# Performance work log

Hardware: AMD Instinct MI355X
Metric: run time of the kernel (lower is better)

## Reference

```python
import jax, jax.numpy as jnp
import numpy as np
from jax import lax

KERNEL_EPS = 1e-4   # eps in softmax_kernel
ATTN_EPS = 1e-6     # eps in causal_linear_attention
CHUNK = 64          # chunk length for the causal scan


def softmax_kernel(data, projection_matrix, is_query):
    # data: [b,h,n,d], projection_matrix: [r,d]
    d = data.shape[-1]
    r = projection_matrix.shape[0]
    data_normalizer = d ** -0.25
    ratio = r ** -0.5
    data_dash = jnp.einsum('bhnd,rd->bhnr', data_normalizer * data, projection_matrix)
    diag_data = (jnp.sum(data ** 2, axis=-1) * 0.5 * data_normalizer ** 2)[..., None]  # [b,h,n,1]
    if is_query:
        stab = jnp.max(data_dash, axis=-1, keepdims=True)
    else:
        stab = jnp.max(data_dash)
    return ratio * (jnp.exp(data_dash - diag_data - stab) + KERNEL_EPS)


def causal_linear_attention(qp, kp, v, chunk=CHUNK, eps=ATTN_EPS):
    # qp,kp: [b,h,n,r] feature maps; v: [b,h,n,e]
    b, h, n, r = qp.shape
    e = v.shape[-1]
    nc = n // chunk
    # -> [nc, b, h, chunk, *] for lax.scan over chunks
    qs = jnp.moveaxis(qp.reshape(b, h, nc, chunk, r), 2, 0)
    ks = jnp.moveaxis(kp.reshape(b, h, nc, chunk, r), 2, 0)
    vs = jnp.moveaxis(v.reshape(b, h, nc, chunk, e), 2, 0)

    def step(carry, xs):
        k_last, ctx_last = carry  # [b,h,r], [b,h,r,e]
        qch, kch, vch = xs        # [b,h,c,r], [b,h,c,r], [b,h,c,e]
        k_cum = k_last[:, :, None, :] + jnp.cumsum(kch, axis=2)              # [b,h,c,r]
        D_inv = 1.0 / jnp.einsum('bhcr,bhcr->bhc', qch, k_cum + eps)         # [b,h,c]
        ctx = jnp.einsum('bhcr,bhce->bhcre', kch, vch)                       # [b,h,c,r,e]
        ctx_cum = ctx_last[:, :, None] + jnp.cumsum(ctx, axis=2)             # [b,h,c,r,e]
        out = jnp.einsum('bhcre,bhcr,bhc->bhce', ctx_cum, qch, D_inv)        # [b,h,c,e]
        return (k_cum[:, :, -1], ctx_cum[:, :, -1]), out

    init = (jnp.zeros((b, h, r), qp.dtype), jnp.zeros((b, h, r, e), qp.dtype))
    _, outs = lax.scan(step, init, (qs, ks, vs))  # outs: [nc,b,h,c,e]
    return jnp.moveaxis(outs, 0, 2).reshape(b, h, n, e)


def setup_inputs() -> dict:
    key = jax.random.key(0)
    kq, kk, kv, kp = jax.random.split(key, 4)
    b, h, n, d, r = 2, 8, 4096, 64, 256
    q = jax.random.normal(kq, (b, h, n, d), dtype=jnp.float32)
    k = jax.random.normal(kk, (b, h, n, d), dtype=jnp.float32)
    v = jax.random.normal(kv, (b, h, n, d), dtype=jnp.float32)
    projection_matrix = jax.random.normal(kp, (r, d), dtype=jnp.float32)
    return {"q": q, "k": k, "v": v, "projection_matrix": projection_matrix}


def reference(q, k, v, projection_matrix):
    qp = softmax_kernel(q, projection_matrix, is_query=True)
    kp = softmax_kernel(k, projection_matrix, is_query=False)
    return causal_linear_attention(qp, kp, v)
```

## Files before the change

### kernel.cpp

```cpp
#include <hip/hip_runtime.h>


typedef unsigned short ushort_t;
typedef __attribute__((ext_vector_type(8))) short bf16x8;
typedef __attribute__((ext_vector_type(4))) float f32x4;

#define KEPS 1e-4f
#define AEPS 1e-6f
#define NORMIZER 0.35355339059327373f
#define RATIO 0.0625f

__device__ __forceinline__ ushort_t bf16r(float f) {
  unsigned u = __float_as_uint(f);
  return (ushort_t)((u + 0x7fffu + ((u >> 16) & 1u)) >> 16);
}
__device__ __forceinline__ float ubf(ushort_t h) {
  return __uint_as_float((unsigned)h << 16);
}

__global__ __launch_bounds__(256) void pconv_kernel(
    const float* __restrict__ P, ushort_t* __restrict__ Phi,
    ushort_t* __restrict__ Plo)
{
  int idx = blockIdx.x * 1024 + threadIdx.x;
  #pragma unroll
  for (int p = 0; p < 4; ++p) {
    int i = idx + p * 256;
    float x = P[i];
    ushort_t h = bf16r(x);
    Phi[i] = h;
    Plo[i] = bf16r(x - ubf(h));
  }
}

__device__ __forceinline__ void stage_ptile(const ushort_t* __restrict__ gt,
                                            ushort_t* lds0, int tid) {
  int wv = tid >> 6, lane = tid & 63;
  #pragma unroll
  for (int i = 0; i < 2; ++i) {
    int D = i * 256 + wv * 64 + lane;
    int row = D >> 3, c3 = D & 7;
    int sc = (row << 3) | (c3 ^ (row & 7));
    __builtin_amdgcn_global_load_lds(
        (const __attribute__((address_space(1))) void*)(gt + sc * 8),
        (__attribute__((address_space(3))) void*)(lds0 + (i * 256 + wv * 64) * 8),
        16, 0, 0);
  }
}

__global__ __launch_bounds__(256, 4) void feat_mfma(
    const float* __restrict__ Q, const float* __restrict__ K,
    const float* __restrict__ V,
    const ushort_t* __restrict__ Phi, const ushort_t* __restrict__ Plo,
    ushort_t* __restrict__ qp, ushort_t* __restrict__ E,
    float* __restrict__ bmax,
    ushort_t* __restrict__ SE, float* __restrict__ zE,
    float* __restrict__ SV)
{
  __shared__ union {
    struct {
      ushort_t Xhi[64 * 72];
      ushort_t Xlo[64 * 72];
      ushort_t Pt[2][4096];
    } s;
    ushort_t outb[64 * 268];
    ushort_t Et[256 * 72];
  } u;
  __shared__ float diagS[64];
  __shared__ float redm[4];

  int bid = blockIdx.x, tid = threadIdx.x;
  bool isK = bid < 1024;
  int bc = bid;
  const float* X = isK ? K : Q;
  size_t rowbase = (size_t)(isK ? bid : bid - 1024) * 64;

  int lane = tid & 63, wv = tid >> 6;
  int n15 = lane & 15, quad = lane >> 4;

  stage_ptile(Phi, &u.s.Pt[0][0], tid);

  float vraw[16];
  if (isK) {
    #pragma unroll
    for (int ks = 0; ks < 2; ++ks)
      #pragma unroll
      for (int jj = 0; jj < 8; ++jj) {
        int pos = quad * 8 + 32 * ks + jj;
        vraw[ks * 8 + jj] = V[rowbase * 64 + (size_t)pos * 64 + 16 * wv + n15];
      }
  }

  #pragma unroll
  for (int p = 0; p < 4; ++p) {
    int idx = tid + p * 256;
    int row = idx >> 4, c4 = idx & 15;
    float4 x = *(const float4*)&X[(rowbase + row) * 64 + c4 * 4];
    ushort4 h, l;
    h.x = bf16r(x.x); l.x = bf16r(x.x - ubf(h.x));
    h.y = bf16r(x.y); l.y = bf16r(x.y - ubf(h.y));
    h.z = bf16r(x.z); l.z = bf16r(x.z - ubf(h.z));
    h.w = bf16r(x.w); l.w = bf16r(x.w - ubf(h.w));
    *(ushort4*)&u.s.Xhi[row * 72 + c4 * 4] = h;
    *(ushort4*)&u.s.Xlo[row * 72 + c4 * 4] = l;
    float ss = x.x * x.x + x.y * x.y + x.z * x.z + x.w * x.w;
    ss += __shfl_xor(ss, 1, 64); ss += __shfl_xor(ss, 2, 64);
    ss += __shfl_xor(ss, 4, 64); ss += __shfl_xor(ss, 8, 64);
    if ((tid & 15) == 0) diagS[row] = 0.0625f * ss;
  }

  bf16x8 aV[2];
  if (isK) {
    float vsum = 0.f;
    #pragma unroll
    for (int ks = 0; ks < 2; ++ks)
      #pragma unroll
      for (int jj = 0; jj < 8; ++jj) {
        float x = vraw[ks * 8 + jj];
        vsum += x;
        aV[ks][jj] = (short)bf16r(x);
      }
    vsum += __shfl_xor(vsum, 16, 64);
    vsum += __shfl_xor(vsum, 32, 64);
    if (quad == 0) SV[(size_t)bc * 64 + 16 * wv + n15] = vsum;
  }

  __syncthreads();

  bf16x8 ah[2], al[2];
  #pragma unroll
  for (int ks = 0; ks < 2; ++ks) {
    int off = (16 * wv + n15) * 72 + quad * 8 + 32 * ks;
    ah[ks] = *(const bf16x8*)&u.s.Xhi[off];
    al[ks] = *(const bf16x8*)&u.s.Xlo[off];
  }

  f32x4 acc[16];
  #pragma unroll
  for (int tc = 0; tc < 16; ++tc) acc[tc] = f32x4{0.f, 0.f, 0.f, 0.f};

  int buf = 0;
  #pragma unroll
  for (int t = 0; t < 8; ++t) {
    int q4 = t >> 1;
    bool isLo = t & 1;
    if (t) {
      asm volatile("s_waitcnt vmcnt(0)" ::: "memory");
      __builtin_amdgcn_s_barrier();
    }
    if (t < 7) {
      int tn = t + 1;
      const ushort_t* gt = ((tn & 1) ? Plo : Phi) + (size_t)(tn >> 1) * 4096;
      stage_ptile(gt, &u.s.Pt[buf ^ 1][0], tid);
    }
    #pragma unroll
    for (int tcl = 0; tcl < 4; ++tcl) {
      f32x4 a = acc[q4 * 4 + tcl];
      #pragma unroll
      for (int ks = 0; ks < 2; ++ks) {
        int jr = 16 * tcl + n15;
        int rc = (quad + 4 * ks) ^ (n15 & 7);
        bf16x8 b = *(const bf16x8*)&u.s.Pt[buf][jr * 64 + rc * 8];
        a = __builtin_amdgcn_mfma_f32_16x16x32_bf16(ah[ks], b, a, 0, 0, 0);
        if (!isLo)
          a = __builtin_amdgcn_mfma_f32_16x16x32_bf16(al[ks], b, a, 0, 0, 0);
      }
      acc[q4 * 4 + tcl] = a;
    }
    buf ^= 1;
  }

  float dg[4];
  #pragma unroll
  for (int r = 0; r < 4; ++r) dg[r] = diagS[16 * wv + quad * 4 + r];

  float sub[4];
  if (!isK) {
    #pragma unroll
    for (int r = 0; r < 4; ++r) {
      float mx = -3.0e38f;
      #pragma unroll
      for (int tc = 0; tc < 16; ++tc) mx = fmaxf(mx, acc[tc][r]);
      #pragma unroll
      for (int s = 1; s < 16; s <<= 1) mx = fmaxf(mx, __shfl_xor(mx, s, 64));
      sub[r] = dg[r] + NORMIZER * mx;
    }
  } else {
    float bm = -3.0e38f;
    #pragma unroll
    for (int tc = 0; tc < 16; ++tc)
      #pragma unroll
      for (int r = 0; r < 4; ++r) bm = fmaxf(bm, acc[tc][r]);
    #pragma unroll
    for (int s = 1; s < 64; s <<= 1) bm = fmaxf(bm, __shfl_xor(bm, s, 64));
    if (lane == 0) redm[wv] = bm;
    #pragma unroll
    for (int r = 0; r < 4; ++r) sub[r] = dg[r];
  }

  unsigned hp[16][2];
  __syncthreads();
  ushort_t* dst = (isK ? E : qp) + rowbase * 256;
  #pragma unroll
  for (int tc = 0; tc < 16; ++tc) {
    #pragma unroll
    for (int r = 0; r < 4; ++r) {
      int row = 16 * wv + quad * 4 + r;
      float ex = __expf(NORMIZER * acc[tc][r] - sub[r]);
      float val = isK ? ex : RATIO * (ex + KEPS);
      ushort_t h = bf16r(val);
      u.outb[row * 268 + 16 * tc + n15] = h;
      if (r & 1) hp[tc][r >> 1] |= ((unsigned)h << 16);
      else       hp[tc][r >> 1] = (unsigned)h;
    }
  }
  __syncthreads();
  #pragma unroll
  for (int p = 0; p < 8; ++p) {
    int g = (tid + p * 256) * 8;
    int row = g >> 8, c0 = g & 255;
    bf16x8 v0 = *(const bf16x8*)&u.outb[row * 268 + c0];
    *(bf16x8*)&dst[row * 256 + c0] = v0;
  }

  if (isK && tid == 0) {
    float m4 = fmaxf(fmaxf(redm[0], redm[1]), fmaxf(redm[2], redm[3]));
    bmax[bc] = NORMIZER * m4;
  }

  if (!isK) return;

  __syncthreads();

  #pragma unroll
  for (int tc = 0; tc < 16; ++tc) {
    int j = 16 * tc + n15;
    int rot = 8 * ((j >> 3) & 7);
    int pw = (16 * wv + quad * 4 + rot) & 63;
    ushort4 w4;
    w4.x = (ushort_t)(hp[tc][0] & 0xffffu);
    w4.y = (ushort_t)(hp[tc][0] >> 16);
    w4.z = (ushort_t)(hp[tc][1] & 0xffffu);
    w4.w = (ushort_t)(hp[tc][1] >> 16);
    *(ushort4*)&u.Et[j * 72 + pw] = w4;
  }
  __syncthreads();

  {
    float s = 0.f;
    #pragma unroll
    for (int m8 = 0; m8 < 8; ++m8) {
      bf16x8 r8 = *(const bf16x8*)&u.Et[tid * 72 + m8 * 8];
      #pragma unroll
      for (int x = 0; x < 8; ++x) s += ubf((ushort_t)r8[x]);
    }
    zE[(size_t)bc * 256 + tid] = s;
  }

  f32x4 acc2[16];
  #pragma unroll
  for (int tc = 0; tc < 16; ++tc) {
    int j = 16 * tc + n15;
    int rot = 8 * ((j >> 3) & 7);
    f32x4 a = {0.f, 0.f, 0.f, 0.f};
    #pragma unroll
    for (int ks = 0; ks < 2; ++ks) {
      int pr = (quad * 8 + 32 * ks + rot) & 63;
      bf16x8 b = *(const bf16x8*)&u.Et[j * 72 + pr];
      a = __builtin_amdgcn_mfma_f32_16x16x32_bf16(aV[ks], b, a, 0, 0, 0);
    }
    acc2[tc] = a;
  }
  __syncthreads();

  #pragma unroll
  for (int tc = 0; tc < 16; ++tc)
    #pragma unroll
    for (int r = 0; r < 4; ++r) {
      int e = 16 * wv + quad * 4 + r;
      u.outb[e * 268 + 16 * tc + n15] = bf16r(acc2[tc][r]);
    }
  __syncthreads();
  ushort_t* sdst = SE + rowbase * 256;
  #pragma unroll
  for (int p = 0; p < 8; ++p) {
    int g = (tid + p * 256) * 8;
    int e = g >> 8, j0 = g & 255;
    bf16x8 v0 = *(const bf16x8*)&u.outb[e * 268 + j0];
    *(bf16x8*)&sdst[e * 256 + j0] = v0;
  }
}

__global__ __launch_bounds__(256) void kmax_reduce(
    const float* __restrict__ bmax, float* __restrict__ kmax)
{
  __shared__ float red[4];
  int tid = threadIdx.x;
  float m = fmaxf(fmaxf(bmax[tid], bmax[tid + 256]),
                  fmaxf(bmax[tid + 512], bmax[tid + 768]));
  #pragma unroll
  for (int s = 1; s < 64; s <<= 1) m = fmaxf(m, __shfl_xor(m, s, 64));
  if ((tid & 63) == 0) red[tid >> 6] = m;
  __syncthreads();
  if (tid == 0)
    *kmax = fmaxf(fmaxf(red[0], red[1]), fmaxf(red[2], red[3]));
}

__global__ __launch_bounds__(256) void prefix_kernel(
    ushort_t* __restrict__ S, float* __restrict__ zE,
    const float* __restrict__ SV, const float* __restrict__ kmax)
{
  int b = blockIdx.x;
  float m = *kmax;
  float c1 = RATIO * __expf(-m);
  const float c0 = RATIO * KEPS;
  if (b < 1024) {
    int flat = b * 256 + threadIdx.x;
    int bh = flat >> 14;
    int idx = flat & 16383;
    int e = idx >> 8;
    size_t base = (size_t)bh * 1048576 + idx;
    const float* svp = SV + (size_t)bh * 4096 + e;
    float runE = 0.f, runV = 0.f;
    for (int cc = 0; cc < 64; cc += 8) {
      ushort_t t[8]; float sv[8];
      #pragma unroll
      for (int u2 = 0; u2 < 8; ++u2) {
        t[u2] = S[base + (size_t)(cc + u2) * 16384];
        sv[u2] = svp[(size_t)(cc + u2) * 64];
      }
      #pragma unroll
      for (int u2 = 0; u2 < 8; ++u2) {
        S[base + (size_t)(cc + u2) * 16384] = bf16r(c1 * runE + c0 * runV);
        runE += ubf(t[u2]);
        runV += sv[u2];
      }
    }
  } else {
    int bh = b - 1024;
    int j = threadIdx.x;
    size_t base = (size_t)bh * 16384 + j;
    float run = 0.f;
    for (int cc = 0; cc < 64; cc += 8) {
      float t[8];
      #pragma unroll
      for (int u2 = 0; u2 < 8; ++u2)
        t[u2] = zE[base + (size_t)(cc + u2) * 256];
      #pragma unroll
      for (int u2 = 0; u2 < 8; ++u2) {
        zE[base + (size_t)(cc + u2) * 256] = run;
        run += c1 * t[u2] + 64.0f * c0;
      }
    }
  }
}

__device__ __forceinline__ void stage_tile(const ushort_t* __restrict__ gt,
                                           ushort_t* lds0, int tid, int wv) {
  #pragma unroll
  for (int i = 0; i < 2; ++i) {
    int D = i * 256 + tid;
    int row = D >> 5, cl = D & 31;
    int sc = (row << 5) | (cl ^ (row & 7));
    __builtin_amdgcn_global_load_lds(
        (const __attribute__((address_space(1))) void*)(gt + sc * 8),
        (__attribute__((address_space(3))) void*)(lds0 + (i * 256 + wv * 64) * 8),
        16, 0, 0);
  }
}

__global__ __launch_bounds__(256) void fused_mfma(
    const ushort_t* __restrict__ qp, const ushort_t* __restrict__ E,
    const float* __restrict__ kmax, const float* __restrict__ Z,
    const ushort_t* __restrict__ S, const float* __restrict__ V,
    float* __restrict__ out)
{
  __shared__ ushort_t As[64 * 72];
  __shared__ ushort_t Vt[64 * 72];
  __shared__ ushort_t Bst[2][4096];
  __shared__ float zv[256];
  __shared__ float qsumS[64];
  __shared__ float dqS[64];

  int bc = blockIdx.x, tid = threadIdx.x;
  int lane = tid & 63, wv = tid >> 6;
  int n15 = lane & 15, quad = lane >> 4;
  float m = *kmax;
  float c1 = RATIO * __expf(-m);
  const float c0 = RATIO * KEPS;
  size_t base = (size_t)bc * 16384;

  zv[tid] = Z[(size_t)bc * 256 + tid] + AEPS;
  #pragma unroll
  for (int p = 0; p < 16; ++p) {
    int idx = tid + p * 256;
    int t = idx >> 6, e = idx & 63;
    Vt[e * 72 + t] = bf16r(V[(size_t)bc * 4096 + idx]);
  }
  __syncthreads();

  stage_tile(E + base, &Bst[0][0], tid, wv);

  bf16x8 aQ[8];
  #pragma unroll
  for (int ks = 0; ks < 8; ++ks)
    aQ[ks] = *(const bf16x8*)&qp[base + (size_t)(16 * wv + n15) * 256 + quad * 8 + 32 * ks];

  float qsum = 0.f, dq = 0.f;
  #pragma unroll
  for (int ks = 0; ks < 8; ++ks)
    #pragma unroll
    for (int j = 0; j < 8; ++j) {
      float qv = ubf((ushort_t)aQ[ks][j]);
      qsum += qv;
      dq += qv * zv[quad * 8 + 32 * ks + j];
    }
  qsum += __shfl_xor(qsum, 16, 64); qsum += __shfl_xor(qsum, 32, 64);
  dq   += __shfl_xor(dq, 16, 64);   dq   += __shfl_xor(dq, 32, 64);
  if (quad == 0) { qsumS[16 * wv + n15] = qsum; dqS[16 * wv + n15] = dq; }

  float rs[4] = {0.f, 0.f, 0.f, 0.f};
  float dinv[4] = {0.f, 0.f, 0.f, 0.f};

  #pragma unroll
  for (int t = 0; t < 8; ++t) {
    asm volatile("s_waitcnt vmcnt(0)" ::: "memory");
    __builtin_amdgcn_s_barrier();
    if (t < 7) {
      const ushort_t* gt = (t < 3) ? (E + base + (size_t)(t + 1) * 4096)
                                   : (S + base + (size_t)(t - 3) * 4096);
      stage_tile(gt, &Bst[(t + 1) & 1][0], tid, wv);
    }

    bf16x8 bf[8];
    #pragma unroll
    for (int ks = 0; ks < 8; ++ks) {
      int rc = (4 * ks + quad) ^ (n15 & 7);
      bf[ks] = *(const bf16x8*)&Bst[t & 1][(n15 * 32 + rc) * 8];
    }
    f32x4 g = {0.f, 0.f, 0.f, 0.f};
    #pragma unroll
    for (int ks = 0; ks < 8; ++ks)
      g = __builtin_amdgcn_mfma_f32_16x16x32_bf16(aQ[ks], bf[ks], g, 0, 0, 0);

    if (t < 4) {
      int tc = t;
      #pragma unroll
      for (int r = 0; r < 4; ++r) {
        int i = 16 * wv + quad * 4 + r;
        int tt = 16 * tc + n15;
        float val = (tt <= i) ? (c1 * g[r] + c0 * qsumS[i]) : 0.f;
        As[i * 72 + tt] = bf16r(val);
        rs[r] += val;
      }
      if (t == 3) {
        #pragma unroll
        for (int r = 0; r < 4; ++r) {
          float v2 = rs[r];
          #pragma unroll
          for (int s = 1; s < 16; s <<= 1) v2 += __shfl_xor(v2, s, 64);
          int i = 16 * wv + quad * 4 + r;
          dinv[r] = 1.f / (dqS[i] + v2);
        }
      }
    } else {
      int ec = t - 4;
      f32x4 o = g;
      #pragma unroll
      for (int ks = 0; ks < 2; ++ks) {
        bf16x8 a2 = *(const bf16x8*)&As[(16 * wv + n15) * 72 + quad * 8 + 32 * ks];
        bf16x8 b2 = *(const bf16x8*)&Vt[(16 * ec + n15) * 72 + quad * 8 + 32 * ks];
        o = __builtin_amdgcn_mfma_f32_16x16x32_bf16(a2, b2, o, 0, 0, 0);
      }
      #pragma unroll
      for (int r = 0; r < 4; ++r) {
        int i = 16 * wv + quad * 4 + r;
        out[(size_t)bc * 4096 + (size_t)i * 64 + 16 * ec + n15] = o[r] * dinv[r];
      }
    }
  }
}

extern "C" void kernel_launch(void* const* d_in, const int* in_sizes, int n_in,
                              void* d_out, int out_size, void* d_ws, size_t ws_size,
                              hipStream_t stream)
{
  const float* q = (const float*)d_in[0];
  const float* k = (const float*)d_in[1];
  const float* v = (const float*)d_in[2];
  const float* P = (const float*)d_in[3];
  float* out = (float*)d_out;

  ushort_t* qp  = (ushort_t*)d_ws;
  ushort_t* E   = qp + 16777216;
  ushort_t* S   = E + 16777216;
  float*    zE  = (float*)(S + 16777216);
  float*    SV  = zE + 262144;
  ushort_t* Phi = (ushort_t*)(SV + 65536);
  ushort_t* Plo = Phi + 16384;
  float*    bmax = (float*)(Plo + 16384);
  float*    kmax = bmax + 1024;

  pconv_kernel<<<16, 256, 0, stream>>>(P, Phi, Plo);
  feat_mfma<<<2048, 256, 0, stream>>>(q, k, v, Phi, Plo, qp, E, bmax,
                                      S, zE, SV);
  kmax_reduce<<<1, 256, 0, stream>>>(bmax, kmax);
  prefix_kernel<<<1040, 256, 0, stream>>>(S, zE, SV, kmax);
  fused_mfma<<<1024, 256, 0, stream>>>(qp, E, kmax, zE, S, v, out);
}
```

Baseline: 157.5 us.

## Drop kmax kernel, load X directly to registers, use packed bf16 converts

Removes the single-block kmax_reduce launch and instead has every prefix and fused block recompute the global max from the 1024 per-block maxima. In feat_mfma the X tile now goes straight from global memory into MFMA operand registers instead of passing through LDS as hi/lo arrays. Scalar bf16 rounding is replaced with the hardware v_cvt_pk_bf16_f32 instruction throughout. The intent is to cut a kernel launch and its serialization, LDS traffic and ALU work. The cost is redundant reads of bmax in every block and possibly less coalesced X loads.

```diff
diff --git a/kernel.cpp b/kernel.cpp
--- a/kernel.cpp
+++ b/kernel.cpp
@@ -17,6 +17,12 @@
 __device__ __forceinline__ float ubf(ushort_t h) {
   return __uint_as_float((unsigned)h << 16);
 }
+__device__ __forceinline__ unsigned cvtpk(float lo, float hi) {
+  unsigned r;
+  asm("v_cvt_pk_bf16_f32 %0, %1, %2" : "=v"(r) : "v"(lo), "v"(hi));
+  return r;
+}
+union U32V { unsigned u[4]; bf16x8 v; };
 
 __global__ __launch_bounds__(256) void pconv_kernel(
     const float* __restrict__ P, ushort_t* __restrict__ Phi,
@@ -58,11 +64,7 @@
     float* __restrict__ SV)
 {
   __shared__ union {
-    struct {
-      ushort_t Xhi[64 * 72];
-      ushort_t Xlo[64 * 72];
-      ushort_t Pt[2][4096];
-    } s;
+    ushort_t Pt[2][4096];
     ushort_t outb[64 * 268];
     ushort_t Et[256 * 72];
   } u;
@@ -78,7 +80,7 @@
   int lane = tid & 63, wv = tid >> 6;
   int n15 = lane & 15, quad = lane >> 4;
 
-  stage_ptile(Phi, &u.s.Pt[0][0], tid);
+  stage_ptile(Phi, &u.Pt[0][0], tid);
 
   float vraw[16];
   if (isK) {
@@ -91,49 +93,64 @@
       }
   }
 
-  #pragma unroll
-  for (int p = 0; p < 4; ++p) {
-    int idx = tid + p * 256;
-    int row = idx >> 4, c4 = idx & 15;
-    float4 x = *(const float4*)&X[(rowbase + row) * 64 + c4 * 4];
-    ushort4 h, l;
-    h.x = bf16r(x.x); l.x = bf16r(x.x - ubf(h.x));
-    h.y = bf16r(x.y); l.y = bf16r(x.y - ubf(h.y));
-    h.z = bf16r(x.z); l.z = bf16r(x.z - ubf(h.z));
-    h.w = bf16r(x.w); l.w = bf16r(x.w - ubf(h.w));
-    *(ushort4*)&u.s.Xhi[row * 72 + c4 * 4] = h;
-    *(ushort4*)&u.s.Xlo[row * 72 + c4 * 4] = l;
-    float ss = x.x * x.x + x.y * x.y + x.z * x.z + x.w * x.w;
-    ss += __shfl_xor(ss, 1, 64); ss += __shfl_xor(ss, 2, 64);
-    ss += __shfl_xor(ss, 4, 64); ss += __shfl_xor(ss, 8, 64);
-    if ((tid & 15) == 0) diagS[row] = 0.0625f * ss;
+  float xr[2][8];
+  {
+    const float* Xr = X + (rowbase + 16 * wv + n15) * 64;
+    #pragma unroll
+    for (int ks = 0; ks < 2; ++ks) {
+      float4 a = *(const float4*)&Xr[quad * 8 + 32 * ks];
+      float4 b = *(const float4*)&Xr[quad * 8 + 32 * ks + 4];
+      xr[ks][0] = a.x; xr[ks][1] = a.y; xr[ks][2] = a.z; xr[ks][3] = a.w;
+      xr[ks][4] = b.x; xr[ks][5] = b.y; xr[ks][6] = b.z; xr[ks][7] = b.w;
+    }
+  }
+  {
+    float ss = 0.f;
+    #pragma unroll
+    for (int ks = 0; ks < 2; ++ks)
+      #pragma unroll
+      for (int j = 0; j < 8; ++j) ss += xr[ks][j] * xr[ks][j];
+    ss += __shfl_xor(ss, 16, 64);
+    ss += __shfl_xor(ss, 32, 64);
+    if (quad == 0) diagS[16 * wv + n15] = 0.0625f * ss;
+  }
+
+  bf16x8 ah[2], al[2];
+  #pragma unroll
+  for (int ks = 0; ks < 2; ++ks) {
+    U32V H, L;
+    #pragma unroll
+    for (int j2 = 0; j2 < 4; ++j2)
+      H.u[j2] = cvtpk(xr[ks][2 * j2], xr[ks][2 * j2 + 1]);
+    #pragma unroll
+    for (int j2 = 0; j2 < 4; ++j2) {
+      float r0 = xr[ks][2 * j2]     - __uint_as_float(H.u[j2] << 16);
+      float r1 = xr[ks][2 * j2 + 1] - __uint_as_float(H.u[j2] & 0xffff0000u);
+      L.u[j2] = cvtpk(r0, r1);
+    }
+    ah[ks] = H.v;
+    al[ks] = L.v;
   }
 
   bf16x8 aV[2];
   if (isK) {
     float vsum = 0.f;
     #pragma unroll
-    for (int ks = 0; ks < 2; ++ks)
-      #pragma unroll
-      for (int jj = 0; jj < 8; ++jj) {
-        float x = vraw[ks * 8 + jj];
-        vsum += x;
-        aV[ks][jj] = (short)bf16r(x);
-      }
+    for (int ks = 0; ks < 2; ++ks) {
+      U32V A;
+      #pragma unroll
+      for (int j2 = 0; j2 < 4; ++j2) {
+        vsum += vraw[ks * 8 + 2 * j2] + vraw[ks * 8 + 2 * j2 + 1];
+        A.u[j2] = cvtpk(vraw[ks * 8 + 2 * j2], vraw[ks * 8 + 2 * j2 + 1]);
+      }
+      aV[ks] = A.v;
+    }
     vsum += __shfl_xor(vsum, 16, 64);
     vsum += __shfl_xor(vsum, 32, 64);
     if (quad == 0) SV[(size_t)bc * 64 + 16 * wv + n15] = vsum;
   }
 
   __syncthreads();
-
-  bf16x8 ah[2], al[2];
-  #pragma unroll
-  for (int ks = 0; ks < 2; ++ks) {
-    int off = (16 * wv + n15) * 72 + quad * 8 + 32 * ks;
-    ah[ks] = *(const bf16x8*)&u.s.Xhi[off];
-    al[ks] = *(const bf16x8*)&u.s.Xlo[off];
-  }
 
   f32x4 acc[16];
   #pragma unroll
@@ -151,7 +168,7 @@
     if (t < 7) {
       int tn = t + 1;
       const ushort_t* gt = ((tn & 1) ? Plo : Phi) + (size_t)(tn >> 1) * 4096;
-      stage_ptile(gt, &u.s.Pt[buf ^ 1][0], tid);
+      stage_ptile(gt, &u.Pt[buf ^ 1][0], tid);
     }
     #pragma unroll
     for (int tcl = 0; tcl < 4; ++tcl) {
@@ -160,7 +177,7 @@
       for (int ks = 0; ks < 2; ++ks) {
         int jr = 16 * tcl + n15;
         int rc = (quad + 4 * ks) ^ (n15 & 7);
-        bf16x8 b = *(const bf16x8*)&u.s.Pt[buf][jr * 64 + rc * 8];
+        bf16x8 b = *(const bf16x8*)&u.Pt[buf][jr * 64 + rc * 8];
         a = __builtin_amdgcn_mfma_f32_16x16x32_bf16(ah[ks], b, a, 0, 0, 0);
         if (!isLo)
           a = __builtin_amdgcn_mfma_f32_16x16x32_bf16(al[ks], b, a, 0, 0, 0);
@@ -204,14 +221,16 @@
   #pragma unroll
   for (int tc = 0; tc < 16; ++tc) {
     #pragma unroll
-    for (int r = 0; r < 4; ++r) {
-      int row = 16 * wv + quad * 4 + r;
-      float ex = __expf(NORMIZER * acc[tc][r] - sub[r]);
-      float val = isK ? ex : RATIO * (ex + KEPS);
-      ushort_t h = bf16r(val);
-      u.outb[row * 268 + 16 * tc + n15] = h;
-      if (r & 1) hp[tc][r >> 1] |= ((unsigned)h << 16);
-      else       hp[tc][r >> 1] = (unsigned)h;
+    for (int rp = 0; rp < 2; ++rp) {
+      float e0 = __expf(NORMIZER * acc[tc][2 * rp]     - sub[2 * rp]);
+      float e1 = __expf(NORMIZER * acc[tc][2 * rp + 1] - sub[2 * rp + 1]);
+      float v0 = isK ? e0 : RATIO * (e0 + KEPS);
+      float v1 = isK ? e1 : RATIO * (e1 + KEPS);
+      unsigned pk = cvtpk(v0, v1);
+      hp[tc][rp] = pk;
+      int row = 16 * wv + quad * 4 + 2 * rp;
+      u.outb[row * 268 + 16 * tc + n15] = (ushort_t)pk;
+      u.outb[(row + 1) * 268 + 16 * tc + n15] = (ushort_t)(pk >> 16);
     }
   }
   __syncthreads();
@@ -276,9 +295,11 @@
   #pragma unroll
   for (int tc = 0; tc < 16; ++tc)
     #pragma unroll
-    for (int r = 0; r < 4; ++r) {
-      int e = 16 * wv + quad * 4 + r;
-      u.outb[e * 268 + 16 * tc + n15] = bf16r(acc2[tc][r]);
+    for (int rp = 0; rp < 2; ++rp) {
+      unsigned pk = cvtpk(acc2[tc][2 * rp], acc2[tc][2 * rp + 1]);
+      int e0 = 16 * wv + quad * 4 + 2 * rp;
+      u.outb[e0 * 268 + 16 * tc + n15] = (ushort_t)pk;
+      u.outb[(e0 + 1) * 268 + 16 * tc + n15] = (ushort_t)(pk >> 16);
     }
   __syncthreads();
   ushort_t* sdst = SE + rowbase * 256;
@@ -291,31 +312,27 @@
   }
 }
 
-__global__ __launch_bounds__(256) void kmax_reduce(
-    const float* __restrict__ bmax, float* __restrict__ kmax)
-{
-  __shared__ float red[4];
-  int tid = threadIdx.x;
-  float m = fmaxf(fmaxf(bmax[tid], bmax[tid + 256]),
-                  fmaxf(bmax[tid + 512], bmax[tid + 768]));
-  #pragma unroll
-  for (int s = 1; s < 64; s <<= 1) m = fmaxf(m, __shfl_xor(m, s, 64));
-  if ((tid & 63) == 0) red[tid >> 6] = m;
-  __syncthreads();
-  if (tid == 0)
-    *kmax = fmaxf(fmaxf(red[0], red[1]), fmaxf(red[2], red[3]));
-}
-
 __global__ __launch_bounds__(256) void prefix_kernel(
     ushort_t* __restrict__ S, float* __restrict__ zE,
-    const float* __restrict__ SV, const float* __restrict__ kmax)
+    const float* __restrict__ SV, const float* __restrict__ bmax)
 {
+  __shared__ float redk[4];
+  int tid = threadIdx.x;
+  {
+    float bm = fmaxf(fmaxf(bmax[tid], bmax[tid + 256]),
+                     fmaxf(bmax[tid + 512], bmax[tid + 768]));
+    #pragma unroll
+    for (int s = 1; s < 64; s <<= 1) bm = fmaxf(bm, __shfl_xor(bm, s, 64));
+    if ((tid & 63) == 0) redk[tid >> 6] = bm;
+  }
+  __syncthreads();
+  float m = fmaxf(fmaxf(redk[0], redk[1]), fmaxf(redk[2], redk[3]));
+
   int b = blockIdx.x;
-  float m = *kmax;
   float c1 = RATIO * __expf(-m);
   const float c0 = RATIO * KEPS;
   if (b < 1024) {
-    int flat = b * 256 + threadIdx.x;
+    int flat = b * 256 + tid;
     int bh = flat >> 14;
     int idx = flat & 16383;
     int e = idx >> 8;
@@ -338,7 +355,7 @@
     }
   } else {
     int bh = b - 1024;
-    int j = threadIdx.x;
+    int j = tid;
     size_t base = (size_t)bh * 16384 + j;
     float run = 0.f;
     for (int cc = 0; cc < 64; cc += 8) {
@@ -371,7 +388,7 @@
 
 __global__ __launch_bounds__(256) void fused_mfma(
     const ushort_t* __restrict__ qp, const ushort_t* __restrict__ E,
-    const float* __restrict__ kmax, const float* __restrict__ Z,
+    const float* __restrict__ bmax, const float* __restrict__ Z,
     const ushort_t* __restrict__ S, const float* __restrict__ V,
     float* __restrict__ out)
 {
@@ -381,15 +398,21 @@
   __shared__ float zv[256];
   __shared__ float qsumS[64];
   __shared__ float dqS[64];
+  __shared__ float redk[4];
 
   int bc = blockIdx.x, tid = threadIdx.x;
   int lane = tid & 63, wv = tid >> 6;
   int n15 = lane & 15, quad = lane >> 4;
-  float m = *kmax;
-  float c1 = RATIO * __expf(-m);
   const float c0 = RATIO * KEPS;
   size_t base = (size_t)bc * 16384;
 
+  {
+    float bm = fmaxf(fmaxf(bmax[tid], bmax[tid + 256]),
+                     fmaxf(bmax[tid + 512], bmax[tid + 768]));
+    #pragma unroll
+    for (int s = 1; s < 64; s <<= 1) bm = fmaxf(bm, __shfl_xor(bm, s, 64));
+    if (lane == 0) redk[wv] = bm;
+  }
   zv[tid] = Z[(size_t)bc * 256 + tid] + AEPS;
   #pragma unroll
   for (int p = 0; p < 16; ++p) {
@@ -398,6 +421,8 @@
     Vt[e * 72 + t] = bf16r(V[(size_t)bc * 4096 + idx]);
   }
   __syncthreads();
+  float m = fmaxf(fmaxf(redk[0], redk[1]), fmaxf(redk[2], redk[3]));
+  float c1 = RATIO * __expf(-m);
 
   stage_tile(E + base, &Bst[0][0], tid, wv);
 
@@ -446,12 +471,16 @@
     if (t < 4) {
       int tc = t;
       #pragma unroll
-      for (int r = 0; r < 4; ++r) {
-        int i = 16 * wv + quad * 4 + r;
+      for (int rp = 0; rp < 2; ++rp) {
+        int i0 = 16 * wv + quad * 4 + 2 * rp;
         int tt = 16 * tc + n15;
-        float val = (tt <= i) ? (c1 * g[r] + c0 * qsumS[i]) : 0.f;
-        As[i * 72 + tt] = bf16r(val);
-        rs[r] += val;
+        float v0 = (tt <= i0)     ? (c1 * g[2 * rp]     + c0 * qsumS[i0])     : 0.f;
+        float v1 = (tt <= i0 + 1) ? (c1 * g[2 * rp + 1] + c0 * qsumS[i0 + 1]) : 0.f;
+        unsigned pk = cvtpk(v0, v1);
+        As[i0 * 72 + tt] = (ushort_t)pk;
+        As[(i0 + 1) * 72 + tt] = (ushort_t)(pk >> 16);
+        rs[2 * rp] += v0;
+        rs[2 * rp + 1] += v1;
       }
       if (t == 3) {
         #pragma unroll
@@ -499,12 +528,10 @@
   ushort_t* Phi = (ushort_t*)(SV + 65536);
   ushort_t* Plo = Phi + 16384;
   float*    bmax = (float*)(Plo + 16384);
-  float*    kmax = bmax + 1024;
 
   pconv_kernel<<<16, 256, 0, stream>>>(P, Phi, Plo);
   feat_mfma<<<2048, 256, 0, stream>>>(q, k, v, Phi, Plo, qp, E, bmax,
                                       S, zE, SV);
-  kmax_reduce<<<1, 256, 0, stream>>>(bmax, kmax);
-  prefix_kernel<<<1040, 256, 0, stream>>>(S, zE, SV, kmax);
-  fused_mfma<<<1024, 256, 0, stream>>>(qp, E, kmax, zE, S, v, out);
-}
+  prefix_kernel<<<1040, 256, 0, stream>>>(S, zE, SV, bmax);
+  fused_mfma<<<1024, 256, 0, stream>>>(qp, E, bmax, zE, S, v, out);
+}
```

New measurement: 153.4 us. 2.6% less time.
